# Kernel optimization log

Hardware: AMD Instinct MI355X
Metric: run time of the kernel (lower is better)

## Reference

```python
import jax, jax.numpy as jnp
import numpy as np

N = [40000, 120000, 80000, 20000]   # simplices per rank 0..3
C = 128
OUT = 10
L = 2
ADJ_NNZ = [320000, 960000, 640000, 160000]
INC_NNZ = [240000, 240000, 80000]   # incidence ranks 1..3


def setup_inputs() -> dict:
    key = jax.random.key(0)
    ki = iter(jax.random.split(key, 40))
    inp = {}
    for r in range(4):
        inp[f"x{r}"] = jax.random.normal(next(ki), (N[r], C), dtype=jnp.float32)
    for r in range(4):
        inp[f"adj{r}_row"] = jax.random.randint(next(ki), (ADJ_NNZ[r],), 0, N[r], dtype=jnp.int32)
        inp[f"adj{r}_col"] = jax.random.randint(next(ki), (ADJ_NNZ[r],), 0, N[r], dtype=jnp.int32)
        inp[f"adj{r}_val"] = jax.random.normal(next(ki), (ADJ_NNZ[r],), dtype=jnp.float32) * 0.1
    for r in range(1, 4):
        nnz = INC_NNZ[r - 1]
        inp[f"inc{r}_row"] = jax.random.randint(next(ki), (nnz,), 0, N[r - 1], dtype=jnp.int32)
        inp[f"inc{r}_col"] = jax.random.randint(next(ki), (nnz,), 0, N[r], dtype=jnp.int32)
        inp[f"inc{r}_val"] = jax.random.normal(next(ki), (nnz,), dtype=jnp.float32) * 0.1
    s = 1.0 / np.sqrt(C).astype(np.float32)
    inp["W_same"] = jax.random.normal(next(ki), (L, 4, C, C), dtype=jnp.float32) * s
    inp["W_h2l"] = jax.random.normal(next(ki), (L, 3, C, C), dtype=jnp.float32) * s
    inp["W_l2h"] = jax.random.normal(next(ki), (L, 3, C, C), dtype=jnp.float32) * s
    inp["W_out"] = jax.random.normal(next(ki), (C, OUT), dtype=jnp.float32) * s
    inp["b_out"] = jnp.zeros((OUT,), dtype=jnp.float32)
    return inp


def _spmm(row, col, val, x, n_rows):
    # y[i] = sum_{k: row[k]==i} val[k] * x[col[k]]   (sparse COO @ dense)
    return jax.ops.segment_sum(val[:, None] * x[col], row, num_segments=n_rows)


def _sccn_forward(xs, adj, inc, W_same, W_h2l, W_l2h):
    for l in range(L):
        new_xs = []
        for r in range(4):
            row, col, val = adj[r]
            m = _spmm(row, col, val, xs[r] @ W_same[l, r], N[r])
            if r < 3:  # high-to-low: incidence_{r+1} @ (x_{r+1} W)
                irow, icol, ival = inc[r]
                m = m + _spmm(irow, icol, ival, xs[r + 1] @ W_h2l[l, r], N[r])
            if r > 0:  # low-to-high: incidence_r^T @ (x_{r-1} W)
                irow, icol, ival = inc[r - 1]
                m = m + _spmm(icol, irow, ival, xs[r - 1] @ W_l2h[l, r - 1], N[r])
            new_xs.append(jax.nn.sigmoid(m))  # update_func='sigmoid' after sum-aggregation
        xs = new_xs
    return xs


def reference(x0, x1, x2, x3,
              adj0_row, adj0_col, adj0_val,
              adj1_row, adj1_col, adj1_val,
              adj2_row, adj2_col, adj2_val,
              adj3_row, adj3_col, adj3_val,
              inc1_row, inc1_col, inc1_val,
              inc2_row, inc2_col, inc2_val,
              inc3_row, inc3_col, inc3_val,
              W_same, W_h2l, W_l2h, W_out, b_out):
    adj = [(adj0_row, adj0_col, adj0_val), (adj1_row, adj1_col, adj1_val),
           (adj2_row, adj2_col, adj2_val), (adj3_row, adj3_col, adj3_val)]
    inc = [(inc1_row, inc1_col, inc1_val), (inc2_row, inc2_col, inc2_val),
           (inc3_row, inc3_col, inc3_val)]
    xs = _sccn_forward([x0, x1, x2, x3], adj, inc, W_same, W_h2l, W_l2h)
    logits = xs[0] @ W_out + b_out
    return jax.nn.softmax(logits, axis=1)
```

## Files before the change

### kernel.cpp

```cpp
#include <hip/hip_runtime.h>

#define CH 128
#define EPB 2048
#define RPB 512
#define MAXBUK 1024
#define MAXBLK 2048

typedef __attribute__((ext_vector_type(8))) short short8;
typedef __attribute__((ext_vector_type(4))) float floatx4;

__device__ __forceinline__ float bf2f(unsigned short u) {
    union { unsigned int i; float f; } v; v.i = ((unsigned int)u) << 16; return v.f;
}
__device__ __forceinline__ unsigned short f2bf(float f) {
    union { float f; unsigned int i; } v; v.f = f;
    unsigned int r = v.i + 0x7FFF + ((v.i >> 16) & 1);
    return (unsigned short)(r >> 16);
}


__global__ __launch_bounds__(256) void k_copy16(const int4* __restrict__ s, int4* __restrict__ d, int n16) {
    int i = blockIdx.x * 256 + threadIdx.x;
    if (i < n16) d[i] = s[i];
}

__global__ __launch_bounds__(256) void k_wt_all(const float* __restrict__ Ws,
                                                const float* __restrict__ Wh,
                                                const float* __restrict__ Wl,
                                                unsigned short* __restrict__ WT) {
    int i = blockIdx.x * 256 + threadIdx.x;
    if (i >= (20 << 14)) return;
    int mat = i >> 14, rem = i & 16383;
    int k = rem >> 7, n = rem & 127;
    float w;
    if (mat < 8)       w = Ws[(mat << 14) + rem];
    else if (mat < 14) w = Wh[((mat - 8) << 14) + rem];
    else               w = Wl[((mat - 14) << 14) + rem];
    WT[(mat << 14) + (n << 7) + k] = f2bf(w);
}


struct Segs {
    const int*   row[10];
    const int*   col[10];
    const float* val[10];
    int base[10];
    int coff[10];
    int nnz[10];
    int start[10];
};

__device__ __forceinline__ int seg_of(const Segs& sg, int blk) {
    int s = 0;
    for (int k = 1; k < 10; ++k) if (blk >= sg.start[k]) s = k;
    return s;
}

__global__ __launch_bounds__(256) void k_bkt_count(Segs sg, int nbuk, int* __restrict__ M) {
    __shared__ int lcnt[MAXBUK];
    int s = seg_of(sg, blockIdx.x);
    int t = threadIdx.x;
    int b0 = (blockIdx.x - sg.start[s]) * EPB;
    int nnz = sg.nnz[s];
    const int* __restrict__ rowp = sg.row[s];
    int sbase = sg.base[s];
    for (int j = t; j < nbuk; j += 256) lcnt[j] = 0;
    __syncthreads();
#pragma unroll
    for (int k = 0; k < 8; ++k) {
        int i = b0 + k * 256 + t;
        if (i < nnz) atomicAdd(&lcnt[(sbase + rowp[i]) >> 9], 1);
    }
    __syncthreads();
    int* Mr = M + (size_t)blockIdx.x * nbuk;
    for (int j = t; j < nbuk; j += 256) Mr[j] = lcnt[j];
}

__global__ __launch_bounds__(256) void k_colscan(int* __restrict__ M, int nblk, int nbuk,
                                                 int* __restrict__ colsum) {
    __shared__ int a[2][MAXBLK];
    int b = blockIdx.x, t = threadIdx.x;
    for (int j = t; j < MAXBLK; j += 256) a[0][j] = (j < nblk) ? M[(size_t)j * nbuk + b] : 0;
    __syncthreads();
    int src = 0;
    for (int off = 1; off < MAXBLK; off <<= 1) {
        for (int j = t; j < MAXBLK; j += 256) {
            int v = a[src][j];
            if (j >= off) v += a[src][j - off];
            a[src ^ 1][j] = v;
        }
        __syncthreads();
        src ^= 1;
    }
    for (int j = t; j < nblk; j += 256)
        M[(size_t)j * nbuk + b] = (j == 0) ? 0 : a[src][j - 1];
    if (t == 0) colsum[b] = a[src][nblk - 1];
}

__global__ __launch_bounds__(256) void k_bkt_scan(const int* __restrict__ colsum, int nbuk,
                                                  int* __restrict__ bucketBase,
                                                  int* __restrict__ rowptr_last) {
    __shared__ int a[2][MAXBUK];
    int t = threadIdx.x;
    for (int j = t; j < MAXBUK; j += 256) a[0][j] = (j < nbuk) ? colsum[j] : 0;
    __syncthreads();
    int src = 0;
    for (int off = 1; off < MAXBUK; off <<= 1) {
        for (int j = t; j < MAXBUK; j += 256) {
            int v = a[src][j];
            if (j >= off) v += a[src][j - off];
            a[src ^ 1][j] = v;
        }
        __syncthreads();
        src ^= 1;
    }
    for (int j = t; j < nbuk; j += 256) bucketBase[j] = (j == 0) ? 0 : a[src][j - 1];
    if (t == 0) { bucketBase[nbuk] = a[src][nbuk - 1]; *rowptr_last = a[src][nbuk - 1]; }
}

__global__ __launch_bounds__(256) void k_bkt_scatter(Segs sg, int nbuk,
                                                     const int* __restrict__ M,
                                                     const int* __restrict__ bucketBase,
                                                     int2* __restrict__ bcv) {
    __shared__ int lcnt[MAXBUK];
    __shared__ int lbase[MAXBUK];
    int s = seg_of(sg, blockIdx.x);
    int t = threadIdx.x;
    int b0 = (blockIdx.x - sg.start[s]) * EPB;
    int nnz = sg.nnz[s];
    const int* __restrict__ rowp = sg.row[s];
    const int* __restrict__ colp = sg.col[s];
    const float* __restrict__ valp = sg.val[s];
    int sbase = sg.base[s];
    int scoff = sg.coff[s];
    for (int j = t; j < nbuk; j += 256) lcnt[j] = 0;
    __syncthreads();
    int rank[8], grow[8];
#pragma unroll
    for (int k = 0; k < 8; ++k) {
        int i = b0 + k * 256 + t;
        if (i < nnz) {
            grow[k] = sbase + rowp[i];
            rank[k] = atomicAdd(&lcnt[grow[k] >> 9], 1);
        }
    }
    __syncthreads();
    const int* Mr = M + (size_t)blockIdx.x * nbuk;
    for (int j = t; j < nbuk; j += 256) lbase[j] = bucketBase[j] + Mr[j];
    __syncthreads();
#pragma unroll
    for (int k = 0; k < 8; ++k) {
        int i = b0 + k * 256 + t;
        if (i < nnz) {
            int pos = lbase[grow[k] >> 9] + rank[k];
            int packed = ((grow[k] & (RPB - 1)) << 19) | (colp[i] + scoff);
            bcv[pos] = make_int2(packed, __float_as_int(valp[i]));
        }
    }
}

__global__ __launch_bounds__(256) void k_bkt_csr(const int2* __restrict__ bcv,
                                                 const int* __restrict__ bucketBase,
                                                 int* __restrict__ rowptr, int totalRows,
                                                 int2* __restrict__ edg) {
    __shared__ int ptr[RPB];
    __shared__ int swt[4];
    int b = blockIdx.x, t = threadIdx.x;
    int bb = bucketBase[b], be = bucketBase[b + 1];
    int bsz = be - bb;
    int rowLo = b << 9;
    for (int j = t; j < RPB; j += 256) ptr[j] = 0;
    __syncthreads();
    for (int i = t; i < bsz; i += 256)
        atomicAdd(&ptr[((unsigned)bcv[bb + i].x) >> 19], 1);
    __syncthreads();
    int base2 = t * 2;
    int c[2];
    int s = 0;
#pragma unroll
    for (int k = 0; k < 2; ++k) { c[k] = ptr[base2 + k]; s += c[k]; }
    int lane = t & 63, w = t >> 6;
    int incl = s;
    for (int off = 1; off < 64; off <<= 1) {
        int u = __shfl_up(incl, off, 64);
        if (lane >= off) incl += u;
    }
    if (lane == 63) swt[w] = incl;
    __syncthreads();
    int waveoff = 0;
    for (int k = 0; k < w; ++k) waveoff += swt[k];
    int run = waveoff + incl - s;
    int nrv = totalRows - rowLo; if (nrv > RPB) nrv = RPB;
#pragma unroll
    for (int k = 0; k < 2; ++k) {
        int j = base2 + k;
        ptr[j] = run;
        if (j < nrv) rowptr[rowLo + j] = bb + run;
        run += c[k];
    }
    __syncthreads();
    for (int i = t; i < bsz; i += 256) {
        int2 e = bcv[bb + i];
        int lrow = ((unsigned)e.x) >> 19;
        int pos = atomicAdd(&ptr[lrow], 1);
        edg[bb + pos] = make_int2(e.x & 0x7FFFF, e.y);
    }
}


__device__ __forceinline__ int lds_idx(int r, int koff) {
    return (r << 7) + ((((koff >> 3) ^ (r & 15))) << 3);
}

__device__ __forceinline__ void gemm_core(const unsigned short* sA, const unsigned short* sB,
                                          unsigned short* __restrict__ Y, int M, int row0, int t) {
    const int wave = t >> 6;
    const int lane = t & 63;
    const int quad = lane >> 4;
    const int l16  = lane & 15;
    const int rbase = wave * 32;

    floatx4 acc[2][8];
    for (int i = 0; i < 2; ++i)
        for (int j = 0; j < 8; ++j) acc[i][j] = (floatx4){0.f, 0.f, 0.f, 0.f};

    for (int kk = 0; kk < 4; ++kk) {
        int ko = kk * 32 + quad * 8;
        short8 a0 = *(const short8*)(&sA[lds_idx(rbase + l16, ko)]);
        short8 a1 = *(const short8*)(&sA[lds_idx(rbase + 16 + l16, ko)]);
        for (int j = 0; j < 8; ++j) {
            short8 b = *(const short8*)(&sB[lds_idx(j * 16 + l16, ko)]);
            acc[0][j] = __builtin_amdgcn_mfma_f32_16x16x32_bf16(a0, b, acc[0][j], 0, 0, 0);
            acc[1][j] = __builtin_amdgcn_mfma_f32_16x16x32_bf16(a1, b, acc[1][j], 0, 0, 0);
        }
    }

    for (int i = 0; i < 2; ++i) {
        int rg0 = row0 + rbase + i * 16 + quad * 4;
        for (int reg = 0; reg < 4; ++reg) {
            int rg = rg0 + reg;
            if (rg >= M) continue;
            unsigned short* yr = Y + (size_t)rg * CH;
            for (int j = 0; j < 8; ++j)
                yr[j * 16 + l16] = f2bf(acc[i][j][reg]);
        }
    }
}

__global__ __launch_bounds__(256) void k_gemm(const unsigned short* __restrict__ A,
                                              const unsigned short* __restrict__ Bt,
                                              unsigned short* __restrict__ Y, int M) {
    __shared__ __align__(16) unsigned short sA[128 * 128];
    __shared__ __align__(16) unsigned short sB[128 * 128];
    const int t = threadIdx.x;
    const int row0 = blockIdx.x * 128;

    for (int it = 0; it < 8; ++it) {
        int chunk = it * 256 + t;
        int r = chunk >> 4;
        int cidx = chunk & 15;
        int coff = cidx << 3;
        int sidx = (r << 7) + (((cidx ^ (r & 15))) << 3);
        *(float4*)(&sB[sidx]) = *(const float4*)(Bt + (r << 7) + coff);
        int gr = row0 + r;
        float4 av = make_float4(0.f, 0.f, 0.f, 0.f);
        if (gr < M) av = *(const float4*)(A + (size_t)gr * CH + coff);
        *(float4*)(&sA[sidx]) = av;
    }
    __syncthreads();
    gemm_core(sA, sB, Y, M, row0, t);
}

__global__ __launch_bounds__(256) void k_gemm_f32(const float* __restrict__ A,
                                                  const unsigned short* __restrict__ Bt,
                                                  unsigned short* __restrict__ Y, int M) {
    __shared__ __align__(16) unsigned short sA[128 * 128];
    __shared__ __align__(16) unsigned short sB[128 * 128];
    const int t = threadIdx.x;
    const int row0 = blockIdx.x * 128;

    for (int it = 0; it < 8; ++it) {
        int chunk = it * 256 + t;
        int r = chunk >> 4;
        int cidx = chunk & 15;
        int coff = cidx << 3;
        int sidx = (r << 7) + (((cidx ^ (r & 15))) << 3);
        *(float4*)(&sB[sidx]) = *(const float4*)(Bt + (r << 7) + coff);
        int gr = row0 + r;
        unsigned short us[8];
        if (gr < M) {
            const float* ar = A + (size_t)gr * CH + coff;
            float4 f0 = *(const float4*)ar;
            float4 f1 = *(const float4*)(ar + 4);
            us[0] = f2bf(f0.x); us[1] = f2bf(f0.y); us[2] = f2bf(f0.z); us[3] = f2bf(f0.w);
            us[4] = f2bf(f1.x); us[5] = f2bf(f1.y); us[6] = f2bf(f1.z); us[7] = f2bf(f1.w);
        } else {
            for (int k = 0; k < 8; ++k) us[k] = 0;
        }
        *(float4*)(&sA[sidx]) = *(const float4*)us;
    }
    __syncthreads();
    gemm_core(sA, sB, Y, M, row0, t);
}


__device__ __forceinline__ void g_load(const int2* __restrict__ eg, int j, int n,
                                       const unsigned short* __restrict__ y, int coff,
                                       int2* e, unsigned int* u) {
#pragma unroll
    for (int k = 0; k < 8; ++k) {
        if (k < n) {
            e[k] = eg[j + k];
            u[k] = *(const unsigned int*)(y + (((size_t)(unsigned)e[k].x) << 7) + coff);
        }
    }
}

__device__ __forceinline__ void g_acc(const int2* e, const unsigned int* u, int n,
                                      float& a0, float& a1) {
#pragma unroll
    for (int k = 0; k < 8; ++k) {
        if (k < n) {
            float v = __int_as_float(e[k].y);
            a0 += v * __int_as_float(u[k] << 16);
            a1 += v * __int_as_float(u[k] & 0xffff0000u);
        }
    }
}

__global__ __launch_bounds__(256) void k_gather(
    const int* __restrict__ rp, const unsigned short* __restrict__ y,
    const int2* __restrict__ eArena,
    unsigned short* __restrict__ xout, int M)
{
    int wrow = blockIdx.x * 4 + (threadIdx.x >> 6);
    if (wrow >= M) return;
    wrow = __builtin_amdgcn_readfirstlane(wrow);
    int lane = threadIdx.x & 63;
    int coff = lane * 2;
    float a0 = 0.f, a1 = 0.f;

    int jb = __builtin_amdgcn_readfirstlane(rp[wrow]);
    int je = __builtin_amdgcn_readfirstlane(rp[wrow + 1]);
    int j = jb;
    int2 ea[8]; unsigned int ua[8];
    int2 eb[8]; unsigned int ub[8];
    int n0 = je - j; if (n0 > 8) n0 = 8;
    if (n0 > 0) g_load(eArena, j, n0, y, coff, ea, ua);
    j += n0;
    while (j < je) {
        int n1 = je - j; if (n1 > 8) n1 = 8;
        g_load(eArena, j, n1, y, coff, eb, ub);
        j += n1;
        g_acc(ea, ua, n0, a0, a1);
#pragma unroll
        for (int k = 0; k < 8; ++k) {
            if (k < n1) { ea[k] = eb[k]; ua[k] = ub[k]; }
        }
        n0 = n1;
    }
    if (n0 > 0) g_acc(ea, ua, n0, a0, a1);

    float s0 = 1.0f / (1.0f + __expf(-a0));
    float s1 = 1.0f / (1.0f + __expf(-a1));
    ushort2 o;
    o.x = f2bf(s0);
    o.y = f2bf(s1);
    *(ushort2*)(xout + (size_t)wrow * CH + coff) = o;
}


__global__ __launch_bounds__(128) void k_out(const unsigned short* __restrict__ x0,
                                             const float* __restrict__ Wout,
                                             const float* __restrict__ bout,
                                             float* __restrict__ out, int M) {
    __shared__ float sl[8][16];
    int rlocal = threadIdx.x >> 4;
    int o = threadIdx.x & 15;
    int rowi = blockIdx.x * 8 + rlocal;
    float acc = 0.f;
    if (rowi < M && o < 10) {
        const unsigned short* xr = x0 + (size_t)rowi * CH;
        for (int k = 0; k < CH; ++k)
            acc += bf2f(xr[k]) * Wout[k * 10 + o];
        acc += bout[o];
    }
    sl[rlocal][o] = acc;
    __syncthreads();
    if (rowi < M && o < 10) {
        float mx = -1e30f;
        for (int j = 0; j < 10; ++j) mx = fmaxf(mx, sl[rlocal][j]);
        float s = 0.f;
        for (int j = 0; j < 10; ++j) s += __expf(sl[rlocal][j] - mx);
        out[rowi * 10 + o] = __expf(sl[rlocal][o] - mx) / s;
    }
}


extern "C" void kernel_launch(void* const* d_in, const int* in_sizes, int n_in,
                              void* d_out, int out_size, void* d_ws, size_t ws_size,
                              hipStream_t stream) {
    const float* xin[4];
    for (int r = 0; r < 4; ++r) xin[r] = (const float*)d_in[r];
    const int* arow[4]; const int* acol[4]; const float* aval[4];
    for (int r = 0; r < 4; ++r) {
        arow[r] = (const int*)d_in[4 + 3 * r];
        acol[r] = (const int*)d_in[5 + 3 * r];
        aval[r] = (const float*)d_in[6 + 3 * r];
    }
    const int* irow[3]; const int* icol[3]; const float* ival[3];
    for (int r = 0; r < 3; ++r) {
        irow[r] = (const int*)d_in[16 + 3 * r];
        icol[r] = (const int*)d_in[17 + 3 * r];
        ival[r] = (const float*)d_in[18 + 3 * r];
    }
    const float* W_same = (const float*)d_in[25];
    const float* W_h2l  = (const float*)d_in[26];
    const float* W_l2h  = (const float*)d_in[27];
    const float* W_out  = (const float*)d_in[28];
    const float* b_out  = (const float*)d_in[29];

    int Nr[4], adjnnz[4], incnnz[3];
    for (int r = 0; r < 4; ++r) { Nr[r] = in_sizes[r] / CH; adjnnz[r] = in_sizes[4 + 3 * r]; }
    for (int r = 0; r < 3; ++r) incnnz[r] = in_sizes[16 + 3 * r];
    int Nmax = 0;
    for (int r = 0; r < 4; ++r) if (Nr[r] > Nmax) Nmax = Nr[r];
    size_t totalN = (size_t)Nr[0] + Nr[1] + Nr[2] + Nr[3];
    size_t totAdj = 0; for (int r = 0; r < 4; ++r) totAdj += adjnnz[r];
    size_t totInc = 0; for (int r = 0; r < 3; ++r) totInc += incnnz[r];
    size_t totEdges = totAdj + 2 * totInc;

    int baseRank[4];
    int acc_rows = 0;
    for (int r = 0; r < 4; ++r) { baseRank[r] = acc_rows; acc_rows += Nr[r]; }
    int totalRowsU = acc_rows;
    int nbuk = (totalRowsU + RPB - 1) >> 9;

    char* ws = (char*)d_ws;
    size_t off = 0;
    auto take = [&](size_t bytes) { char* p = ws + off; off += (bytes + 255) & ~(size_t)255; return p; };
    unsigned short* xbuf  = (unsigned short*)take(totalN * CH * 2);
    unsigned short* xsave = (unsigned short*)take((size_t)Nmax * CH * 2);
    unsigned short* yS    = (unsigned short*)take((size_t)3 * Nmax * CH * 2);
    unsigned short* WT    = (unsigned short*)take((size_t)20 * 16384 * 2);
    int*  rowptrG= (int*)take(((size_t)totalRowsU + 1) * 4);
    int2* eArena = (int2*)take(totEdges * 8);
    (void)ws_size;

    unsigned short* yH = yS + (size_t)Nmax * CH;
    unsigned short* yL = yS + (size_t)2 * Nmax * CH;

    unsigned short* WsT = WT;
    unsigned short* WhT = WT + ((size_t)8 << 14);
    unsigned short* WlT = WT + ((size_t)14 << 14);

    unsigned short* x[4];
    {
        size_t o = 0;
        for (int r = 0; r < 4; ++r) { x[r] = xbuf + o; o += (size_t)Nr[r] * CH; }
    }

    Segs sg;
    int nblk = 0;
    {
        for (int r = 0; r < 4; ++r) {
            sg.row[r] = arow[r]; sg.col[r] = acol[r]; sg.val[r] = aval[r];
            sg.base[r] = baseRank[r]; sg.coff[r] = 0;
            sg.nnz[r] = adjnnz[r]; sg.start[r] = nblk;
            nblk += (adjnnz[r] + EPB - 1) / EPB;
        }
        for (int s = 0; s < 3; ++s) {
            sg.row[4 + s] = irow[s]; sg.col[4 + s] = icol[s]; sg.val[4 + s] = ival[s];
            sg.base[4 + s] = baseRank[s]; sg.coff[4 + s] = Nmax;
            sg.nnz[4 + s] = incnnz[s]; sg.start[4 + s] = nblk;
            nblk += (incnnz[s] + EPB - 1) / EPB;
        }
        for (int s = 0; s < 3; ++s) {
            sg.row[7 + s] = icol[s]; sg.col[7 + s] = irow[s]; sg.val[7 + s] = ival[s];
            sg.base[7 + s] = baseRank[s + 1]; sg.coff[7 + s] = 2 * Nmax;
            sg.nnz[7 + s] = incnnz[s]; sg.start[7 + s] = nblk;
            nblk += (incnnz[s] + EPB - 1) / EPB;
        }

        int2* bcv  = (int2*)yS;
        int*  M    = (int*)yL;
        int*  colsum     = M + (size_t)nblk * nbuk;
        int*  bucketBase = colsum + nbuk;

        k_bkt_count  <<<nblk, 256, 0, stream>>>(sg, nbuk, M);
        k_colscan    <<<nbuk, 256, 0, stream>>>(M, nblk, nbuk, colsum);
        k_bkt_scan   <<<1,    256, 0, stream>>>(colsum, nbuk, bucketBase, rowptrG + totalRowsU);
        k_bkt_scatter<<<nblk, 256, 0, stream>>>(sg, nbuk, M, bucketBase, bcv);
        k_bkt_csr    <<<nbuk, 256, 0, stream>>>(bcv, bucketBase, rowptrG, totalRowsU, eArena);
    }

    k_wt_all<<<(20 * 16384 + 255) / 256, 256, 0, stream>>>(W_same, W_h2l, W_l2h, WT);

    for (int l = 0; l < 2; ++l) {
        for (int r = 0; r < 4; ++r) {
            int M = Nr[r];
            const unsigned short* bS = WsT + (((size_t)(l * 4 + r)) << 14);
            if (l == 0) k_gemm_f32<<<(M + 127) / 128, 256, 0, stream>>>(xin[r], bS, yS, M);
            else        k_gemm    <<<(M + 127) / 128, 256, 0, stream>>>(x[r],   bS, yS, M);
            if (r < 3) {
                int Ms = Nr[r + 1];
                const unsigned short* bH = WhT + (((size_t)(l * 3 + r)) << 14);
                if (l == 0) k_gemm_f32<<<(Ms + 127) / 128, 256, 0, stream>>>(xin[r + 1], bH, yH, Ms);
                else        k_gemm    <<<(Ms + 127) / 128, 256, 0, stream>>>(x[r + 1],   bH, yH, Ms);
            }
            if (r > 0) {
                int Ms = Nr[r - 1];
                const unsigned short* bL = WlT + (((size_t)(l * 3 + r - 1)) << 14);
                if (l == 0) k_gemm_f32<<<(Ms + 127) / 128, 256, 0, stream>>>(xin[r - 1], bL, yL, Ms);
                else        k_gemm    <<<(Ms + 127) / 128, 256, 0, stream>>>(xsave,      bL, yL, Ms);
            }
            if (l == 1 && r < 3) {
                int n16 = M * 16;
                k_copy16<<<(n16 + 255) / 256, 256, 0, stream>>>((const int4*)x[r], (int4*)xsave, n16);
            }
            k_gather<<<(M + 3) / 4, 256, 0, stream>>>(
                rowptrG + baseRank[r], yS, eArena, x[r], M);
        }
    }

    k_out<<<(Nr[0] + 7) / 8, 128, 0, stream>>>(x[0], W_out, b_out, (float*)d_out, Nr[0]);
}
```

Before: 947.8 us.

## Batch per-rank GEMMs into one multi-job launch and compute l2h eagerly

Merges the same-rank, high-to-low and low-to-high GEMMs for each rank into a single launch that picks its job from the block index. The low-to-high product for rank r+1 is now computed from x[r] before x[r] is overwritten and stored in one of two ping-pong buffers. This removes the xsave copy kernel and its buffer. It cuts kernel launches and gives the GPU larger grids, at the cost of one extra Nmax-sized workspace slot and edge column offsets that alternate by rank parity.

```diff
diff --git a/kernel.cpp b/kernel.cpp
--- a/kernel.cpp
+++ b/kernel.cpp
@@ -18,11 +18,6 @@
     return (unsigned short)(r >> 16);
 }
 
-
-__global__ __launch_bounds__(256) void k_copy16(const int4* __restrict__ s, int4* __restrict__ d, int n16) {
-    int i = blockIdx.x * 256 + threadIdx.x;
-    if (i < n16) d[i] = s[i];
-}
 
 __global__ __launch_bounds__(256) void k_wt_all(const float* __restrict__ Ws,
                                                 const float* __restrict__ Wh,
@@ -247,13 +242,28 @@
     }
 }
 
-__global__ __launch_bounds__(256) void k_gemm(const unsigned short* __restrict__ A,
-                                              const unsigned short* __restrict__ Bt,
-                                              unsigned short* __restrict__ Y, int M) {
+struct GJobs {
+    const void* A[3];
+    const unsigned short* Bt[3];
+    unsigned short* Y[3];
+    int M[3];
+    int bstart[4];
+    int njobs;
+};
+
+__global__ __launch_bounds__(256) void k_gemm_multi(GJobs g) {
     __shared__ __align__(16) unsigned short sA[128 * 128];
     __shared__ __align__(16) unsigned short sB[128 * 128];
     const int t = threadIdx.x;
-    const int row0 = blockIdx.x * 128;
+    int b = blockIdx.x;
+    int j = 0;
+    if (g.njobs > 1 && b >= g.bstart[1]) j = 1;
+    if (g.njobs > 2 && b >= g.bstart[2]) j = 2;
+    const unsigned short* A = (const unsigned short*)g.A[j];
+    const unsigned short* Bt = g.Bt[j];
+    unsigned short* Y = g.Y[j];
+    int M = g.M[j];
+    const int row0 = (b - g.bstart[j]) * 128;
 
     for (int it = 0; it < 8; ++it) {
         int chunk = it * 256 + t;
@@ -271,13 +281,19 @@
     gemm_core(sA, sB, Y, M, row0, t);
 }
 
-__global__ __launch_bounds__(256) void k_gemm_f32(const float* __restrict__ A,
-                                                  const unsigned short* __restrict__ Bt,
-                                                  unsigned short* __restrict__ Y, int M) {
+__global__ __launch_bounds__(256) void k_gemm_multi_f32(GJobs g) {
     __shared__ __align__(16) unsigned short sA[128 * 128];
     __shared__ __align__(16) unsigned short sB[128 * 128];
     const int t = threadIdx.x;
-    const int row0 = blockIdx.x * 128;
+    int b = blockIdx.x;
+    int j = 0;
+    if (g.njobs > 1 && b >= g.bstart[1]) j = 1;
+    if (g.njobs > 2 && b >= g.bstart[2]) j = 2;
+    const float* A = (const float*)g.A[j];
+    const unsigned short* Bt = g.Bt[j];
+    unsigned short* Y = g.Y[j];
+    int M = g.M[j];
+    const int row0 = (b - g.bstart[j]) * 128;
 
     for (int it = 0; it < 8; ++it) {
         int chunk = it * 256 + t;
@@ -440,15 +456,16 @@
     size_t off = 0;
     auto take = [&](size_t bytes) { char* p = ws + off; off += (bytes + 255) & ~(size_t)255; return p; };
     unsigned short* xbuf  = (unsigned short*)take(totalN * CH * 2);
-    unsigned short* xsave = (unsigned short*)take((size_t)Nmax * CH * 2);
-    unsigned short* yS    = (unsigned short*)take((size_t)3 * Nmax * CH * 2);
+    unsigned short* yS    = (unsigned short*)take((size_t)4 * Nmax * CH * 2);
     unsigned short* WT    = (unsigned short*)take((size_t)20 * 16384 * 2);
     int*  rowptrG= (int*)take(((size_t)totalRowsU + 1) * 4);
     int2* eArena = (int2*)take(totEdges * 8);
     (void)ws_size;
 
-    unsigned short* yH = yS + (size_t)Nmax * CH;
-    unsigned short* yL = yS + (size_t)2 * Nmax * CH;
+    unsigned short* yH  = yS + (size_t)Nmax * CH;
+    unsigned short* yLe = yS + (size_t)2 * Nmax * CH;
+    unsigned short* yLo = yS + (size_t)3 * Nmax * CH;
+    unsigned short* yLslot[2] = { yLe, yLo };
 
     unsigned short* WsT = WT;
     unsigned short* WhT = WT + ((size_t)8 << 14);
@@ -477,13 +494,14 @@
         }
         for (int s = 0; s < 3; ++s) {
             sg.row[7 + s] = icol[s]; sg.col[7 + s] = irow[s]; sg.val[7 + s] = ival[s];
-            sg.base[7 + s] = baseRank[s + 1]; sg.coff[7 + s] = 2 * Nmax;
+            sg.base[7 + s] = baseRank[s + 1];
+            sg.coff[7 + s] = (2 + ((s + 1) & 1)) * Nmax;
             sg.nnz[7 + s] = incnnz[s]; sg.start[7 + s] = nblk;
             nblk += (incnnz[s] + EPB - 1) / EPB;
         }
 
         int2* bcv  = (int2*)yS;
-        int*  M    = (int*)yL;
+        int*  M    = (int*)yLe;
         int*  colsum     = M + (size_t)nblk * nbuk;
         int*  bucketBase = colsum + nbuk;
 
@@ -498,28 +516,31 @@
 
     for (int l = 0; l < 2; ++l) {
         for (int r = 0; r < 4; ++r) {
-            int M = Nr[r];
-            const unsigned short* bS = WsT + (((size_t)(l * 4 + r)) << 14);
-            if (l == 0) k_gemm_f32<<<(M + 127) / 128, 256, 0, stream>>>(xin[r], bS, yS, M);
-            else        k_gemm    <<<(M + 127) / 128, 256, 0, stream>>>(x[r],   bS, yS, M);
+            GJobs g;
+            int nj = 0;
+            g.A[nj] = (l == 0) ? (const void*)xin[r] : (const void*)x[r];
+            g.Bt[nj] = WsT + (((size_t)(l * 4 + r)) << 14);
+            g.Y[nj] = yS; g.M[nj] = Nr[r];
+            ++nj;
             if (r < 3) {
-                int Ms = Nr[r + 1];
-                const unsigned short* bH = WhT + (((size_t)(l * 3 + r)) << 14);
-                if (l == 0) k_gemm_f32<<<(Ms + 127) / 128, 256, 0, stream>>>(xin[r + 1], bH, yH, Ms);
-                else        k_gemm    <<<(Ms + 127) / 128, 256, 0, stream>>>(x[r + 1],   bH, yH, Ms);
+                g.A[nj] = (l == 0) ? (const void*)xin[r + 1] : (const void*)x[r + 1];
+                g.Bt[nj] = WhT + (((size_t)(l * 3 + r)) << 14);
+                g.Y[nj] = yH; g.M[nj] = Nr[r + 1];
+                ++nj;
+                g.A[nj] = (l == 0) ? (const void*)xin[r] : (const void*)x[r];
+                g.Bt[nj] = WlT + (((size_t)(l * 3 + r)) << 14);
+                g.Y[nj] = yLslot[(r + 1) & 1]; g.M[nj] = Nr[r];
+                ++nj;
             }
-            if (r > 0) {
-                int Ms = Nr[r - 1];
-                const unsigned short* bL = WlT + (((size_t)(l * 3 + r - 1)) << 14);
-                if (l == 0) k_gemm_f32<<<(Ms + 127) / 128, 256, 0, stream>>>(xin[r - 1], bL, yL, Ms);
-                else        k_gemm    <<<(Ms + 127) / 128, 256, 0, stream>>>(xsave,      bL, yL, Ms);
-            }
-            if (l == 1 && r < 3) {
-                int n16 = M * 16;
-                k_copy16<<<(n16 + 255) / 256, 256, 0, stream>>>((const int4*)x[r], (int4*)xsave, n16);
-            }
-            k_gather<<<(M + 3) / 4, 256, 0, stream>>>(
-                rowptrG + baseRank[r], yS, eArena, x[r], M);
+            g.njobs = nj;
+            int bacc = 0;
+            for (int k = 0; k < nj; ++k) { g.bstart[k] = bacc; bacc += (g.M[k] + 127) / 128; }
+            g.bstart[nj] = bacc;
+            if (l == 0) k_gemm_multi_f32<<<bacc, 256, 0, stream>>>(g);
+            else        k_gemm_multi    <<<bacc, 256, 0, stream>>>(g);
+
+            k_gather<<<(Nr[r] + 3) / 4, 256, 0, stream>>>(
+                rowptrG + baseRank[r], yS, eArena, x[r], Nr[r]);
         }
     }
 
```

Measured after the change: 832.9 us. -12.1%, faster.
